# Optimization experiments

Measured on AMD Instinct MI355X. Metric: run time of the kernel, lower is better.

The kernel has to match this reference:

```python
import jax, jax.numpy as jnp
import numpy as np

B, T, I, H = 512, 256, 256, 512


def _lstm(x, Wih, Whh, bih, bhh):
    # x: [B, T, I]; Wih: [4H, I]; Whh: [4H, H]; gate order i, f, g, o (torch)
    Bv = x.shape[0]
    Hv = Whh.shape[1]
    xg = jnp.einsum('bti,gi->btg', x, Wih) + bih + bhh  # [B, T, 4H] (input projections hoisted out of scan)
    xg = jnp.transpose(xg, (1, 0, 2))  # [T, B, 4H]
    h0 = jnp.zeros((Bv, Hv), x.dtype)
    c0 = jnp.zeros((Bv, Hv), x.dtype)

    def step(carry, gx):
        h, c = carry
        g = gx + h @ Whh.T  # [B, 4H]
        i, f, gg, o = jnp.split(g, 4, axis=-1)
        i = jax.nn.sigmoid(i)
        f = jax.nn.sigmoid(f)
        gg = jnp.tanh(gg)
        o = jax.nn.sigmoid(o)
        c = f * c + i * gg
        h = o * jnp.tanh(c)
        return (h, c), h

    _, hs = jax.lax.scan(step, (h0, c0), xg)  # hs: [T, B, H]
    return jnp.transpose(hs, (1, 0, 2))  # [B, T, H]


def _bn1d(x, gamma, beta, eps=1e-5):
    # torch BatchNorm1d on [N, C, L] in training mode: per-channel stats over (N, L), biased var
    m = jnp.mean(x, axis=(0, 2), keepdims=True)
    v = jnp.var(x, axis=(0, 2), keepdims=True)
    return (x - m) * jax.lax.rsqrt(v + eps) * gamma[None, :, None] + beta[None, :, None]


def setup_inputs() -> dict:
    key = jax.random.key(0)
    ks = jax.random.split(key, 14)
    s = 1.0 / np.sqrt(H)
    return {
        'x': jax.random.normal(ks[0], (B, T, I), jnp.float32),
        'Wih': jax.random.uniform(ks[1], (4 * H, I), jnp.float32, -s, s),
        'Whh': jax.random.uniform(ks[2], (4 * H, H), jnp.float32, -s, s),
        'bih': jax.random.uniform(ks[3], (4 * H,), jnp.float32, -s, s),
        'bhh': jax.random.uniform(ks[4], (4 * H,), jnp.float32, -s, s),
        'fc1_w': jax.random.uniform(ks[5], (32, H), jnp.float32, -s, s),
        'fc1_b': jax.random.uniform(ks[6], (32,), jnp.float32, -s, s),
        'fc2_w': jax.random.uniform(ks[7], (1, 32), jnp.float32, -0.17, 0.17),
        'fc2_b': jax.random.uniform(ks[8], (1,), jnp.float32, -0.17, 0.17),
        'bn1_g': jnp.ones((T,), jnp.float32),
        'bn1_b': jnp.zeros((T,), jnp.float32),
        'bn2_g': jnp.ones((T,), jnp.float32),
        'bn2_b': jnp.zeros((T,), jnp.float32),
    }


def reference(x, Wih, Whh, bih, bhh, fc1_w, fc1_b, fc2_w, fc2_b, bn1_g, bn1_b, bn2_g, bn2_b):
    lstm_out = _lstm(x, Wih, Whh, bih, bhh)  # [B, T, H]
    a = jnp.einsum('bth,oh->bto', lstm_out, fc1_w) + fc1_b  # [B, T, 32]
    a = jax.nn.leaky_relu(_bn1d(a, bn1_g, bn1_b), negative_slope=0.1)
    z = jnp.einsum('bto,po->btp', a, fc2_w) + fc2_b  # [B, T, 1]
    out = jax.nn.relu(_bn1d(z, bn2_g, bn2_b))
    return out
```

## Files before the change

### kernel.cpp

```cpp
#include <hip/hip_runtime.h>

#define BB 512
#define TT 256
#define II 256
#define HH 512

typedef __attribute__((ext_vector_type(8))) short bf16x8;
typedef __attribute__((ext_vector_type(4))) float f32x4;

__device__ __forceinline__ unsigned short f2bf(float f) {
  union { float f; unsigned u; } v; v.f = f;
  unsigned r = v.u + 0x7fffu + ((v.u >> 16) & 1u);
  return (unsigned short)(r >> 16);
}

#define OFF_CNT   0
#define OFF_HSWZ  4096
#define OFF_XSWZ  1052672ULL
#define OFF_HIST  68161536ULL
#define ZERO_WORDS 263168

__global__ void zero_k(unsigned* __restrict__ p, int n) {
  int i = blockIdx.x * blockDim.x + threadIdx.x;
  if (i < n) p[i] = 0u;
}

__global__ __launch_bounds__(256) void prep_x(const float* __restrict__ x,
                                              unsigned char* __restrict__ ws) {
  __shared__ unsigned short xs[16][264];
  const int t = blockIdx.x >> 5, rc = blockIdx.x & 31;
  const int tid = threadIdx.x;
  {
    const int r = tid >> 4, seg = tid & 15;
    const float* src = x + ((size_t)(rc * 16 + r) * TT + t) * II + seg * 16;
    const float4* s4 = (const float4*)src;
#pragma unroll
    for (int q = 0; q < 4; ++q) {
      float4 v = s4[q];
      xs[r][seg * 16 + q * 4 + 0] = f2bf(v.x);
      xs[r][seg * 16 + q * 4 + 1] = f2bf(v.y);
      xs[r][seg * 16 + q * 4 + 2] = f2bf(v.z);
      xs[r][seg * 16 + q * 4 + 3] = f2bf(v.w);
    }
  }
  __syncthreads();
  const int lane = tid & 63;
  const int row16 = lane & 15, koff = (lane >> 4) * 8;
#pragma unroll
  for (int kc = tid >> 6; kc < 8; kc += 4) {
    union { unsigned short h[8]; uint4 v; } pk;
#pragma unroll
    for (int j = 0; j < 8; ++j) pk.h[j] = xs[row16][kc * 32 + koff + j];
    *(uint4*)(ws + OFF_XSWZ + (size_t)(t * 8 + kc) * 32768u +
              ((size_t)rc * 64 + lane) * 16) = pk.v;
  }
}

__global__ __launch_bounds__(512, 2) void lstm_persist(
    const float* __restrict__ Wih, const float* __restrict__ Whh,
    const float* __restrict__ bih, const float* __restrict__ bhh,
    unsigned char* __restrict__ ws)
{
  const int gid = blockIdx.x;
  const int group = gid & 7;
  const int m = gid >> 3;
  const int tid = threadIdx.x;
  const int wv = tid >> 6, lane = tid & 63;
  const int mb = wv & 3, kh = wv >> 2;
  const int lq = lane >> 4, ln = lane & 15;

  int* cnt = (int*)(ws + OFF_CNT + (size_t)group * 512);
  unsigned char* xswz  = ws + OFF_XSWZ;
  unsigned char* hswz0 = ws + OFF_HSWZ;
  unsigned char* hswz1 = ws + OFF_HSWZ + 524288;
  unsigned char* hist  = ws + OFF_HIST;

  bf16x8 Wf[12][4];
#pragma unroll
  for (int kk = 0; kk < 12; ++kk) {
    const int kb = (kh * 12 + kk) * 32 + lq * 8;
#pragma unroll
    for (int nt = 0; nt < 4; ++nt) {
      const int gcol = nt * 512 + m * 16 + ln;
      const float* s = (kb < 256) ? (Wih + (size_t)gcol * 256 + kb)
                                  : (Whh + (size_t)gcol * 512 + (kb - 256));
      bf16x8 w;
#pragma unroll
      for (int j = 0; j < 8; ++j) w[j] = (short)f2bf(s[j]);
      Wf[kk][nt] = w;
    }
  }

  float bia[4];
#pragma unroll
  for (int nt = 0; nt < 4; ++nt) {
    int gcol = nt * 512 + m * 16 + ln;
    bia[nt] = bih[gcol] + bhh[gcol];
  }

  __shared__ float g_s[64 * 68];
  __shared__ float h_s[64 * 17];

  const size_t aoff = ((size_t)(group * 4 + mb) * 64 + lane) * 16;
  float creg[4] = {0.f, 0.f, 0.f, 0.f};
  const f32x4 zero4 = {0.f, 0.f, 0.f, 0.f};

#pragma unroll 1
  for (int t = 0; t < 256; ++t) {
    unsigned char* hrd = (t & 1) ? hswz1 : hswz0;
    unsigned char* hwr = (t & 1) ? hswz0 : hswz1;

    f32x4 acc[4] = {zero4, zero4, zero4, zero4};

    if (kh == 0) {
#pragma unroll
      for (int kk = 0; kk < 8; ++kk) {
        bf16x8 a = *(const bf16x8*)(xswz + (size_t)(t * 8 + kk) * 32768u + aoff);
#pragma unroll
        for (int nt = 0; nt < 4; ++nt)
          acc[nt] = __builtin_amdgcn_mfma_f32_16x16x32_bf16(a, Wf[kk][nt], acc[nt], 0, 0, 0);
      }
    }

    if (t > 0) {
      int iter = 0;
      while (__hip_atomic_load(cnt, __ATOMIC_RELAXED, __HIP_MEMORY_SCOPE_AGENT) < t * 32
             && iter < (1 << 17)) { ++iter; __builtin_amdgcn_s_sleep(1); }
    }

    if (kh == 0) {
      unsigned long long u0[4], u1[4];
#pragma unroll
      for (int p = 0; p < 4; ++p) {
        const unsigned long long* q =
            (const unsigned long long*)(hrd + (size_t)p * 32768u + aoff);
        u0[p] = __hip_atomic_load(q + 0, __ATOMIC_RELAXED, __HIP_MEMORY_SCOPE_AGENT);
        u1[p] = __hip_atomic_load(q + 1, __ATOMIC_RELAXED, __HIP_MEMORY_SCOPE_AGENT);
      }
#pragma unroll
      for (int kk = 0; kk < 4; ++kk) {
        union { unsigned long long q[2]; bf16x8 v; } u;
        u.q[0] = u0[kk]; u.q[1] = u1[kk];
#pragma unroll
        for (int nt = 0; nt < 4; ++nt)
          acc[nt] = __builtin_amdgcn_mfma_f32_16x16x32_bf16(u.v, Wf[8 + kk][nt], acc[nt], 0, 0, 0);
      }
    } else {
      unsigned long long u0[6], u1[6];
#pragma unroll
      for (int p = 0; p < 6; ++p) {
        const unsigned long long* q =
            (const unsigned long long*)(hrd + (size_t)(4 + p) * 32768u + aoff);
        u0[p] = __hip_atomic_load(q + 0, __ATOMIC_RELAXED, __HIP_MEMORY_SCOPE_AGENT);
        u1[p] = __hip_atomic_load(q + 1, __ATOMIC_RELAXED, __HIP_MEMORY_SCOPE_AGENT);
      }
#pragma unroll
      for (int kk = 0; kk < 12; ++kk) {
        const int slot = kk % 6;
        union { unsigned long long q[2]; bf16x8 v; } u;
        u.q[0] = u0[slot]; u.q[1] = u1[slot];
        if (kk < 6) {
          const unsigned long long* q =
              (const unsigned long long*)(hrd + (size_t)(10 + kk) * 32768u + aoff);
          u0[slot] = __hip_atomic_load(q + 0, __ATOMIC_RELAXED, __HIP_MEMORY_SCOPE_AGENT);
          u1[slot] = __hip_atomic_load(q + 1, __ATOMIC_RELAXED, __HIP_MEMORY_SCOPE_AGENT);
        }
#pragma unroll
        for (int nt = 0; nt < 4; ++nt)
          acc[nt] = __builtin_amdgcn_mfma_f32_16x16x32_bf16(u.v, Wf[kk][nt], acc[nt], 0, 0, 0);
      }
#pragma unroll
      for (int nt = 0; nt < 4; ++nt)
#pragma unroll
        for (int r = 0; r < 4; ++r)
          g_s[(mb * 16 + lq * 4 + r) * 68 + nt * 16 + ln] = acc[nt][r];
    }
    __syncthreads();

    if (kh == 0) {
#pragma unroll
      for (int r = 0; r < 4; ++r) {
        const int rw = mb * 16 + lq * 4 + r;
        float gi = acc[0][r] + g_s[rw * 68 + ln]      + bia[0];
        float gf = acc[1][r] + g_s[rw * 68 + 16 + ln] + bia[1];
        float gg = acc[2][r] + g_s[rw * 68 + 32 + ln] + bia[2];
        float go = acc[3][r] + g_s[rw * 68 + 48 + ln] + bia[3];
        float iv = 1.f / (1.f + __expf(-gi));
        float fv = 1.f / (1.f + __expf(-gf));
        float gv = 1.f - 2.f / (__expf(2.f * gg) + 1.f);
        float ov = 1.f / (1.f + __expf(-go));
        float cv = fv * creg[r] + iv * gv;
        creg[r] = cv;
        h_s[rw * 17 + ln] = ov * (1.f - 2.f / (__expf(2.f * cv) + 1.f));
      }
    }
    __syncthreads();

    if (tid < 256) {
      {
        int rc_l = tid >> 6;
        int rem = tid & 63;
        int lane_off = rem >> 1;
        int half = rem & 1;
        int l2 = (m & 1) * 32 + lane_off;
        int rowl = rc_l * 16 + (lane_off & 15);
        int jb = (lane_off >> 4) * 8 + half * 4;
        union { ushort4 s; unsigned long long q; } pk;
        pk.s = make_ushort4(f2bf(h_s[rowl * 17 + jb + 0]),
                            f2bf(h_s[rowl * 17 + jb + 1]),
                            f2bf(h_s[rowl * 17 + jb + 2]),
                            f2bf(h_s[rowl * 17 + jb + 3]));
        size_t off = ((size_t)((m >> 1) * 32 + group * 4 + rc_l) * 64 + l2) * 16 + half * 8;
        __hip_atomic_store((unsigned long long*)(hwr + off), pk.q,
                           __ATOMIC_RELAXED, __HIP_MEMORY_SCOPE_AGENT);
      }
      {
        int row = tid >> 2, jb = (tid & 3) * 4;
        ushort4 hq = make_ushort4(f2bf(h_s[row * 17 + jb + 0]),
                                  f2bf(h_s[row * 17 + jb + 1]),
                                  f2bf(h_s[row * 17 + jb + 2]),
                                  f2bf(h_s[row * 17 + jb + 3]));
        int b = group * 64 + row;
        *(ushort4*)(hist + ((size_t)(b * 256 + t) * 512 + m * 16 + jb) * 2) = hq;
      }
    }
    __syncthreads();

    if (tid == 0)
      __hip_atomic_fetch_add(cnt, 1, __ATOMIC_RELAXED, __HIP_MEMORY_SCOPE_AGENT);
  }
}

__global__ __launch_bounds__(256) void e1_fc1(
    const float* __restrict__ fc1_w, const unsigned char* __restrict__ hist,
    float* __restrict__ a_out)
{
  const int tid = threadIdx.x, wv = tid >> 6, lane = tid & 63;
  const int lq = lane >> 4, ln = lane & 15;

  bf16x8 Bf[16][2];
#pragma unroll
  for (int kk = 0; kk < 16; ++kk) {
#pragma unroll
    for (int nt = 0; nt < 2; ++nt) {
      const float* s = fc1_w + (size_t)(nt * 16 + ln) * 512 + kk * 32 + lq * 8;
      bf16x8 w;
#pragma unroll
      for (int j = 0; j < 8; ++j) w[j] = (short)f2bf(s[j]);
      Bf[kk][nt] = w;
    }
  }

  const int rbase = blockIdx.x * 128 + wv * 32;
  const f32x4 zero4 = {0.f, 0.f, 0.f, 0.f};
  f32x4 acc[2][2] = {{zero4, zero4}, {zero4, zero4}};
#pragma unroll
  for (int kk = 0; kk < 16; ++kk) {
    bf16x8 a0 = *(const bf16x8*)(hist + ((size_t)(rbase + ln) * 512 + kk * 32 + lq * 8) * 2);
    bf16x8 a1 = *(const bf16x8*)(hist + ((size_t)(rbase + 16 + ln) * 512 + kk * 32 + lq * 8) * 2);
#pragma unroll
    for (int nt = 0; nt < 2; ++nt) {
      acc[0][nt] = __builtin_amdgcn_mfma_f32_16x16x32_bf16(a0, Bf[kk][nt], acc[0][nt], 0, 0, 0);
      acc[1][nt] = __builtin_amdgcn_mfma_f32_16x16x32_bf16(a1, Bf[kk][nt], acc[1][nt], 0, 0, 0);
    }
  }
#pragma unroll
  for (int mt = 0; mt < 2; ++mt)
#pragma unroll
    for (int nt = 0; nt < 2; ++nt)
#pragma unroll
      for (int r = 0; r < 4; ++r) {
        int row = rbase + mt * 16 + lq * 4 + r;
        a_out[(size_t)row * 32 + nt * 16 + ln] = acc[mt][nt][r];
      }
}

__global__ __launch_bounds__(256) void e2_head(
    const float* __restrict__ a_in, const float* __restrict__ fc1_b,
    const float* __restrict__ fc2_w, const float* __restrict__ fc2_b,
    const float* __restrict__ bn1_g, const float* __restrict__ bn1_b,
    const float* __restrict__ bn2_g, const float* __restrict__ bn2_b,
    float* __restrict__ out)
{
  const int t = blockIdx.x, tid = threadIdx.x;
  __shared__ float fb[32], fw[32];
  __shared__ float red[4][2], red2[4][2];
  if (tid < 32) { fb[tid] = fc1_b[tid]; fw[tid] = fc2_w[tid]; }
  __syncthreads();

  float va[2][32];
  float s1 = 0.f, s2 = 0.f;
#pragma unroll
  for (int rr = 0; rr < 2; ++rr) {
    int b = tid * 2 + rr;
    const float* p = a_in + ((size_t)b * 256 + t) * 32;
#pragma unroll
    for (int o = 0; o < 32; ++o) {
      float v = p[o] + fb[o];
      va[rr][o] = v;
      s1 += v; s2 += v * v;
    }
  }
#pragma unroll
  for (int off = 32; off > 0; off >>= 1) {
    s1 += __shfl_down(s1, off);
    s2 += __shfl_down(s2, off);
  }
  if ((tid & 63) == 0) { red[tid >> 6][0] = s1; red[tid >> 6][1] = s2; }
  __syncthreads();
  float tot1 = red[0][0] + red[1][0] + red[2][0] + red[3][0];
  float tot2 = red[0][1] + red[1][1] + red[2][1] + red[3][1];
  float m1 = tot1 * (1.f / 16384.f);
  float v1 = tot2 * (1.f / 16384.f) - m1 * m1;
  float sc1 = bn1_g[t] * rsqrtf(v1 + 1e-5f);
  float sh1 = bn1_b[t];

  float z[2];
  float zs1 = 0.f, zs2 = 0.f;
#pragma unroll
  for (int rr = 0; rr < 2; ++rr) {
    float acc = fc2_b[0];
#pragma unroll
    for (int o = 0; o < 32; ++o) {
      float av = (va[rr][o] - m1) * sc1 + sh1;
      av = (av > 0.f) ? av : 0.1f * av;
      acc += av * fw[o];
    }
    z[rr] = acc; zs1 += acc; zs2 += acc * acc;
  }
#pragma unroll
  for (int off = 32; off > 0; off >>= 1) {
    zs1 += __shfl_down(zs1, off);
    zs2 += __shfl_down(zs2, off);
  }
  if ((tid & 63) == 0) { red2[tid >> 6][0] = zs1; red2[tid >> 6][1] = zs2; }
  __syncthreads();
  float zt1 = red2[0][0] + red2[1][0] + red2[2][0] + red2[3][0];
  float zt2 = red2[0][1] + red2[1][1] + red2[2][1] + red2[3][1];
  float m2 = zt1 * (1.f / 512.f);
  float v2 = zt2 * (1.f / 512.f) - m2 * m2;
  float sc2 = bn2_g[t] * rsqrtf(v2 + 1e-5f);
  float sh2 = bn2_b[t];
#pragma unroll
  for (int rr = 0; rr < 2; ++rr) {
    int b = tid * 2 + rr;
    float res = (z[rr] - m2) * sc2 + sh2;
    out[(size_t)b * 256 + t] = (res > 0.f) ? res : 0.f;
  }
}

extern "C" void kernel_launch(void* const* d_in, const int* in_sizes, int n_in,
                              void* d_out, int out_size, void* d_ws, size_t ws_size,
                              hipStream_t stream) {
  const float* x    = (const float*)d_in[0];
  const float* Wih  = (const float*)d_in[1];
  const float* Whh  = (const float*)d_in[2];
  const float* bih  = (const float*)d_in[3];
  const float* bhh  = (const float*)d_in[4];
  const float* fc1w = (const float*)d_in[5];
  const float* fc1b = (const float*)d_in[6];
  const float* fc2w = (const float*)d_in[7];
  const float* fc2b = (const float*)d_in[8];
  const float* b1g  = (const float*)d_in[9];
  const float* b1b  = (const float*)d_in[10];
  const float* b2g  = (const float*)d_in[11];
  const float* b2b  = (const float*)d_in[12];
  unsigned char* ws = (unsigned char*)d_ws;
  float* out = (float*)d_out;
  float* a_buf = (float*)(ws + OFF_XSWZ);

  zero_k<<<1028, 256, 0, stream>>>((unsigned*)ws, ZERO_WORDS);
  prep_x<<<8192, 256, 0, stream>>>(x, ws);
  lstm_persist<<<256, 512, 0, stream>>>(Wih, Whh, bih, bhh, ws);
  e1_fc1<<<1024, 256, 0, stream>>>(fc1w, ws + OFF_HIST, a_buf);
  e2_head<<<256, 256, 0, stream>>>(a_buf, fc1b, fc2w, fc2b, b1g, b1b, b2g, b2b, out);
}
```

Before: 1.661 ms.

## Replace shared atomic counter barrier with per-block step flags polled by wavefronts

Replaces the per-group atomic fetch_add counter and the trailing block-wide barrier with one flag per producer block, padded to separate cache lines. Each wave polls all 32 flags with a ballot, and only the writer wave waits on its own stores before publishing. The h-state writeback is moved to a single wave and the history write to another, so the other waves can continue without a second __syncthreads. This targets the serialized atomic contention and the barrier on the recurrent critical path. In exchange it relies on relaxed ordering plus a manual waitcnt for visibility, and it removes a sync whose absence could race h_s reuse in the next step.

Measured after the change: 1.776 ms. +6.9%, slower.

```diff
diff --git a/kernel.cpp b/kernel.cpp
--- a/kernel.cpp
+++ b/kernel.cpp
@@ -14,11 +14,11 @@
   return (unsigned short)(r >> 16);
 }
 
-#define OFF_CNT   0
-#define OFF_HSWZ  4096
-#define OFF_XSWZ  1052672ULL
-#define OFF_HIST  68161536ULL
-#define ZERO_WORDS 263168
+#define OFF_FLAG  0
+#define OFF_HSWZ  32768
+#define OFF_XSWZ  1081344ULL
+#define OFF_HIST  68190208ULL
+#define ZERO_WORDS 270336
 
 __global__ void zero_k(unsigned* __restrict__ p, int n) {
   int i = blockIdx.x * blockDim.x + threadIdx.x;
@@ -53,6 +53,19 @@
     for (int j = 0; j < 8; ++j) pk.h[j] = xs[row16][kc * 32 + koff + j];
     *(uint4*)(ws + OFF_XSWZ + (size_t)(t * 8 + kc) * 32768u +
               ((size_t)rc * 64 + lane) * 16) = pk.v;
+  }
+}
+
+__device__ __forceinline__ void pollwait(const int* flags, int t, int lane) {
+  if (t == 0) return;
+  int iter = 0;
+  for (;;) {
+    int f = 0x7fffffff;
+    if (lane < 32)
+      f = __hip_atomic_load(flags + lane * 32, __ATOMIC_RELAXED, __HIP_MEMORY_SCOPE_AGENT);
+    if (__ballot(f < t) == 0ULL) break;
+    if (++iter > (1 << 17)) break;
+    __builtin_amdgcn_s_sleep(1);
   }
 }
 
@@ -69,7 +82,7 @@
   const int mb = wv & 3, kh = wv >> 2;
   const int lq = lane >> 4, ln = lane & 15;
 
-  int* cnt = (int*)(ws + OFF_CNT + (size_t)group * 512);
+  int* flags = (int*)(ws + OFF_FLAG + (size_t)group * 4096);
   unsigned char* xswz  = ws + OFF_XSWZ;
   unsigned char* hswz0 = ws + OFF_HSWZ;
   unsigned char* hswz1 = ws + OFF_HSWZ + 524288;
@@ -120,15 +133,7 @@
         for (int nt = 0; nt < 4; ++nt)
           acc[nt] = __builtin_amdgcn_mfma_f32_16x16x32_bf16(a, Wf[kk][nt], acc[nt], 0, 0, 0);
       }
-    }
-
-    if (t > 0) {
-      int iter = 0;
-      while (__hip_atomic_load(cnt, __ATOMIC_RELAXED, __HIP_MEMORY_SCOPE_AGENT) < t * 32
-             && iter < (1 << 17)) { ++iter; __builtin_amdgcn_s_sleep(1); }
-    }
-
-    if (kh == 0) {
+      pollwait(flags, t, lane);
       unsigned long long u0[4], u1[4];
 #pragma unroll
       for (int p = 0; p < 4; ++p) {
@@ -146,6 +151,7 @@
           acc[nt] = __builtin_amdgcn_mfma_f32_16x16x32_bf16(u.v, Wf[8 + kk][nt], acc[nt], 0, 0, 0);
       }
     } else {
+      pollwait(flags, t, lane);
       unsigned long long u0[6], u1[6];
 #pragma unroll
       for (int p = 0; p < 6; ++p) {
@@ -196,38 +202,39 @@
     }
     __syncthreads();
 
-    if (tid < 256) {
-      {
-        int rc_l = tid >> 6;
-        int rem = tid & 63;
-        int lane_off = rem >> 1;
-        int half = rem & 1;
+    if (wv == 7) {
+#pragma unroll
+      for (int uu = 0; uu < 2; ++uu) {
+        int u = uu * 64 + lane;
+        int rc_l = u >> 5;
+        int lane_off = u & 31;
         int l2 = (m & 1) * 32 + lane_off;
         int rowl = rc_l * 16 + (lane_off & 15);
-        int jb = (lane_off >> 4) * 8 + half * 4;
-        union { ushort4 s; unsigned long long q; } pk;
-        pk.s = make_ushort4(f2bf(h_s[rowl * 17 + jb + 0]),
-                            f2bf(h_s[rowl * 17 + jb + 1]),
-                            f2bf(h_s[rowl * 17 + jb + 2]),
-                            f2bf(h_s[rowl * 17 + jb + 3]));
-        size_t off = ((size_t)((m >> 1) * 32 + group * 4 + rc_l) * 64 + l2) * 16 + half * 8;
-        __hip_atomic_store((unsigned long long*)(hwr + off), pk.q,
+        int jb0 = (lane_off >> 4) * 8;
+        union { unsigned short h[8]; unsigned long long q[2]; } pk;
+#pragma unroll
+        for (int j = 0; j < 8; ++j) pk.h[j] = f2bf(h_s[rowl * 17 + jb0 + j]);
+        unsigned long long* dst = (unsigned long long*)
+            (hwr + ((size_t)((m >> 1) * 32 + group * 4 + rc_l) * 64 + l2) * 16);
+        __hip_atomic_store(dst + 0, pk.q[0], __ATOMIC_RELAXED, __HIP_MEMORY_SCOPE_AGENT);
+        __hip_atomic_store(dst + 1, pk.q[1], __ATOMIC_RELAXED, __HIP_MEMORY_SCOPE_AGENT);
+      }
+      __builtin_amdgcn_s_waitcnt(0x0F70);
+      if (lane == 0)
+        __hip_atomic_store(flags + m * 32, t + 1,
                            __ATOMIC_RELAXED, __HIP_MEMORY_SCOPE_AGENT);
-      }
-      {
-        int row = tid >> 2, jb = (tid & 3) * 4;
-        ushort4 hq = make_ushort4(f2bf(h_s[row * 17 + jb + 0]),
-                                  f2bf(h_s[row * 17 + jb + 1]),
-                                  f2bf(h_s[row * 17 + jb + 2]),
-                                  f2bf(h_s[row * 17 + jb + 3]));
-        int b = group * 64 + row;
-        *(ushort4*)(hist + ((size_t)(b * 256 + t) * 512 + m * 16 + jb) * 2) = hq;
-      }
-    }
-    __syncthreads();
-
-    if (tid == 0)
-      __hip_atomic_fetch_add(cnt, 1, __ATOMIC_RELAXED, __HIP_MEMORY_SCOPE_AGENT);
+    } else if (wv == 6) {
+      union { unsigned short h[8]; uint4 v; } p0, p1;
+#pragma unroll
+      for (int j = 0; j < 8; ++j) {
+        p0.h[j] = f2bf(h_s[lane * 17 + j]);
+        p1.h[j] = f2bf(h_s[lane * 17 + 8 + j]);
+      }
+      int b = group * 64 + lane;
+      uint4* dst = (uint4*)(hist + ((size_t)(b * 256 + t) * 512 + m * 16) * 2);
+      dst[0] = p0.v;
+      dst[1] = p1.v;
+    }
   }
 }
 
@@ -369,7 +376,7 @@
   float* out = (float*)d_out;
   float* a_buf = (float*)(ws + OFF_XSWZ);
 
-  zero_k<<<1028, 256, 0, stream>>>((unsigned*)ws, ZERO_WORDS);
+  zero_k<<<1056, 256, 0, stream>>>((unsigned*)ws, ZERO_WORDS);
   prep_x<<<8192, 256, 0, stream>>>(x, ws);
   lstm_persist<<<256, 512, 0, stream>>>(Wih, Whh, bih, bhh, ws);
   e1_fc1<<<1024, 256, 0, stream>>>(fc1w, ws + OFF_HIST, a_buf);
```
